# Optimization experiments

Measured on AMD Instinct MI355X. Metric: run time of the kernel, lower is better.

## Reference

```python
import jax, jax.numpy as jnp
import numpy as np

N = 100000   # nodes
E = 1600000  # edges
F_IN = 64    # n_features
H = 32       # hidden_size
OUT = 1      # output_size


def _lin(k, fan_in, fan_out):
    return (jax.random.normal(k, (fan_in, fan_out), jnp.float32) / np.sqrt(fan_in)).astype(jnp.float32)


def setup_inputs() -> dict:
    key = jax.random.key(0)
    ks = jax.random.split(key, 16)
    x = jax.random.normal(ks[0], (N, F_IN), jnp.float32)
    edge_index = jax.random.randint(ks[1], (2, E), 0, N, dtype=jnp.int64)
    # guarantee current_node (=0) has outgoing edges so the legal-move mask is non-empty
    edge_index = edge_index.at[0, :64].set(0)
    edge_attr = jax.random.uniform(ks[2], (E,), jnp.float32)
    return {
        "x": x, "edge_index": edge_index, "edge_attr": edge_attr, "current_node": 0,
        # conv_in: GraphConv(F_IN -> H)
        "Win_rel": _lin(ks[3], F_IN, H), "bin_rel": jnp.zeros((H,), jnp.float32), "Win_root": _lin(ks[4], F_IN, H),
        # conv_hidden: GraphConv(H -> H)
        "Wh_rel": _lin(ks[5], H, H), "bh_rel": jnp.zeros((H,), jnp.float32), "Wh_root": _lin(ks[6], H, H),
        # policy_conv: GraphConv(H -> OUT)
        "Wp_rel": _lin(ks[7], H, OUT), "bp_rel": jnp.zeros((OUT,), jnp.float32), "Wp_root": _lin(ks[8], H, OUT),
        # value_conv: GraphConv(H -> OUT)
        "Wv_rel": _lin(ks[9], H, OUT), "bv_rel": jnp.zeros((OUT,), jnp.float32), "Wv_root": _lin(ks[10], H, OUT),
    }


def _graph_conv(h, src, dst, ew, W_rel, b_rel, W_root):
    # PyG GraphConv: out_i = W_root h_i + W_rel * sum_{j->i} e_ji * h_j + b
    msg = h[src] * ew[:, None]                              # [E, d] gather + scale
    agg = jax.ops.segment_sum(msg, dst, num_segments=N)      # [N, d] scatter-add
    return agg @ W_rel + b_rel + h @ W_root


def reference(x, edge_index, edge_attr, current_node,
              Win_rel, bin_rel, Win_root,
              Wh_rel, bh_rel, Wh_root,
              Wp_rel, bp_rel, Wp_root,
              Wv_rel, bv_rel, Wv_root):
    src, dst = edge_index[0], edge_index[1]
    h = jax.nn.relu(_graph_conv(x, src, dst, edge_attr, Win_rel, bin_rel, Win_root))
    h = jax.nn.relu(_graph_conv(h, src, dst, edge_attr, Wh_rel, bh_rel, Wh_root))
    p = _graph_conv(h, src, dst, edge_attr, Wp_rel, bp_rel, Wp_root)  # [N, 1]
    v = _graph_conv(h, src, dst, edge_attr, Wv_rel, bv_rel, Wv_root)  # [N, 1]
    # illegal_moves_mask: 1 for nodes directly reachable from current_node
    hit = (src == current_node).astype(jnp.float32)
    mask = (jnp.zeros((N,), jnp.float32).at[dst].add(hit) > 0).astype(jnp.float32)
    p_m = mask * p.T                                   # [1, N]
    p_m = jnp.where(p_m == 0, -jnp.inf, p_m)
    p_soft = jax.nn.softmax(p_m, axis=1)
    v_m = mask * v.T                                   # [1, N]
    return p_soft.reshape(-1), v_m.reshape(-1)
```

## Files before the change

kernel.cpp:

```cpp
#include <hip/hip_runtime.h>
#include <hip/hip_fp16.h>
#include <cmath>

static constexpr int NN = 100000;
static constexpr int NE = 1600000;
static const size_t NW = (size_t)NN * 32;
static constexpr int SUB = 256;
static constexpr int NSUB = 391;
static constexpr int CH = 8192;
static constexpr int NCH = (NE + CH - 1) / CH;
static constexpr int BCAP = 5200;
static constexpr int CSRN = NSUB * BCAP;
static constexpr int MCAP = 4096;

__device__ __forceinline__ float ent_w(unsigned e)
{
    return __half2float(__ushort_as_half((unsigned short)(e >> 17)));
}
__device__ __forceinline__ int ent_s(unsigned e)
{
    int s = (int)(e & 0x1FFFF);
    return s < NN ? s : NN - 1;
}

__device__ __forceinline__ float4 pack8(const float* v)
{
    union { __half2 h2[4]; float4 f4; } u;
    u.h2[0] = __floats2half2_rn(v[0], v[1]);
    u.h2[1] = __floats2half2_rn(v[2], v[3]);
    u.h2[2] = __floats2half2_rn(v[4], v[5]);
    u.h2[3] = __floats2half2_rn(v[6], v[7]);
    return u.f4;
}

__device__ __forceinline__ int wave_incl_scan(int v, int lane)
{
    int s = v;
#pragma unroll
    for (int d = 1; d < 64; d <<= 1) {
        int o = __shfl_up(s, d, 64);
        if (lane >= d) s += o;
    }
    return s;
}

__global__ void __launch_bounds__(512) fused_build_mm1_k(
    const int* __restrict__ src, const int* __restrict__ dst,
    const float* __restrict__ ew, const int* __restrict__ curp,
    int* __restrict__ maskb, int* __restrict__ mcount, int* __restrict__ mlist,
    int* __restrict__ bcnt, unsigned* __restrict__ bx,
    unsigned char* __restrict__ bd,
    const float* __restrict__ x, const float* __restrict__ Wrel,
    const float* __restrict__ Wroot, const float* __restrict__ bin,
    __half* __restrict__ proj1, __half* __restrict__ root1)
{
    __shared__ union {
        struct {
            unsigned sBufX[CH];
            unsigned char sBufD[CH];
            int lhist[NSUB];
            int lpos[NSUB];
            int lstart[NSUB];
            int lbase[NSUB];
            int tscan[512];
        } s;
        struct {
            float sX[128 * 65];
            float sW[64 * 68];
        } m;
    } u;

    int t = threadIdx.x;
    int bid = blockIdx.x;

    if (bid < NCH) {
        for (int i = t; i < NSUB; i += 512) { u.s.lhist[i] = 0; u.s.lpos[i] = 0; }
        __syncthreads();
        int c0 = bid * CH;
        int cur = curp[0];
        unsigned rx[CH / 512];
        int rd[CH / 512];
#pragma unroll
        for (int it = 0; it < CH / 512; ++it) {
            int e = c0 + it * 512 + t;
            rd[it] = -1;
            if (e < NE) {
                int d = dst[e];
                int sv = src[e];
                if ((unsigned)d < (unsigned)NN) {
                    rd[it] = d;
                    unsigned bits = __half_as_ushort(__float2half(ew[e]));
                    rx[it] = ((unsigned)sv & 0x1FFFF) | (bits << 17);
                    atomicAdd(&u.s.lhist[d >> 8], 1);
                    if (sv == cur) {
                        if (atomicExch(maskb + d, 1) == 0) {
                            int idx = atomicAdd(mcount, 1);
                            if (idx < MCAP) mlist[idx] = d;
                        }
                    }
                }
            }
        }
        __syncthreads();
        {
            int v = (t < NSUB) ? u.s.lhist[t] : 0;
            int lane = t & 63, wv = t >> 6;
            int sI = wave_incl_scan(v, lane);
            if (lane == 63) u.s.tscan[wv] = sI;
            __syncthreads();
            if (t == 0) {
                int r = 0;
#pragma unroll
                for (int w2 = 0; w2 < 8; ++w2) {
                    int xw = u.s.tscan[w2];
                    u.s.tscan[8 + w2] = r;
                    r += xw;
                }
            }
            __syncthreads();
            if (t < NSUB) {
                u.s.lstart[t] = sI + u.s.tscan[8 + wv] - v;
                u.s.lbase[t] = (v > 0) ? atomicAdd(&bcnt[t], v) : 0;
            }
        }
        __syncthreads();
#pragma unroll
        for (int it = 0; it < CH / 512; ++it) {
            if (rd[it] >= 0) {
                int b = rd[it] >> 8;
                int p = atomicAdd(&u.s.lpos[b], 1);
                int pos = u.s.lstart[b] + p;
                u.s.sBufX[pos] = rx[it];
                u.s.sBufD[pos] = (unsigned char)(rd[it] & 255);
            }
        }
        __syncthreads();
        int grp = t >> 4, l16 = t & 15;
        for (int b = grp; b < NSUB; b += 32) {
            int s0 = u.s.lstart[b];
            int cb = u.s.lhist[b];
            int gb = u.s.lbase[b];
            size_t gb0 = (size_t)b * BCAP;
            for (int j = l16; j < cb; j += 16) {
                unsigned pos = (unsigned)(gb + j);
                if (pos < (unsigned)BCAP) {
                    bx[gb0 + pos] = u.s.sBufX[s0 + j];
                    bd[gb0 + pos] = u.s.sBufD[s0 + j];
                }
            }
        }
    } else {
        int mb = bid - NCH;
        for (int i = t; i < 64 * 32; i += 512) {
            int k = i >> 5, j = i & 31;
            u.m.sW[k * 68 + j] = Wrel[i];
            u.m.sW[k * 68 + 32 + j] = Wroot[i];
        }
        int base = mb * 128;
        for (int i = t; i < 2048; i += 512) {
            int node = i >> 4;
            int k = (i & 15) * 4;
            int n = base + node;
            if (n >= NN) n = NN - 1;
            float4 v4 = *(const float4*)(x + (size_t)n * 64 + k);
            float* p = u.m.sX + node * 65 + k;
            p[0] = v4.x; p[1] = v4.y; p[2] = v4.z; p[3] = v4.w;
        }
        __syncthreads();
        int cg = t & 7;
        int ng = t >> 3;
        int c0m = 8 * cg;
        float acc[2][8] = {};
        for (int k = 0; k < 64; ++k) {
            float xv0 = u.m.sX[(2 * ng + 0) * 65 + k];
            float xv1 = u.m.sX[(2 * ng + 1) * 65 + k];
            float4 w0 = *(const float4*)(u.m.sW + k * 68 + c0m);
            float4 w1 = *(const float4*)(u.m.sW + k * 68 + c0m + 4);
            const float* wp = (const float*)&w0;
#pragma unroll
            for (int j = 0; j < 4; ++j) {
                float w = wp[j];
                acc[0][j] = fmaf(xv0, w, acc[0][j]);
                acc[1][j] = fmaf(xv1, w, acc[1][j]);
            }
            const float* wq = (const float*)&w1;
#pragma unroll
            for (int j = 0; j < 4; ++j) {
                float w = wq[j];
                acc[0][4 + j] = fmaf(xv0, w, acc[0][4 + j]);
                acc[1][4 + j] = fmaf(xv1, w, acc[1][4 + j]);
            }
        }
#pragma unroll
        for (int r = 0; r < 2; ++r) {
            int n = base + 2 * ng + r;
            if (n >= NN) break;
            if (cg < 4) {
                *(float4*)(proj1 + (size_t)n * 32 + c0m) = pack8(acc[r]);
            } else {
                int c = c0m - 32;
                float vv[8];
#pragma unroll
                for (int j = 0; j < 8; ++j) vv[j] = acc[r][j] + bin[c + j];
                *(float4*)(root1 + (size_t)n * 32 + c) = pack8(vv);
            }
        }
    }
}

__global__ void __launch_bounds__(1024) sortagg1_k(
    const unsigned* __restrict__ bx, const unsigned char* __restrict__ bd,
    const int* __restrict__ bcnt,
    const __half* __restrict__ proj1, const __half* __restrict__ root1,
    unsigned* __restrict__ csr4, int* __restrict__ deg, int* __restrict__ off,
    __half* __restrict__ h1)
{
    __shared__ unsigned sX[BCAP];
    __shared__ unsigned char sD[BCAP];
    __shared__ unsigned sE[BCAP];
    __shared__ int lhist[SUB];
    __shared__ int lstart[SUB];
    __shared__ int lcur[SUB];
    __shared__ int tscan[16];
    int g = blockIdx.x, t = threadIdx.x;
    if (t < SUB) { lhist[t] = 0; lcur[t] = 0; }
    __syncthreads();
    int cnt = bcnt[g];
    if (cnt < 0) cnt = 0;
    if (cnt > BCAP) cnt = BCAP;
    size_t gbase = (size_t)g * BCAP;
    for (int i = t; i < cnt; i += 1024) {
        unsigned e = bx[gbase + i];
        unsigned char d = bd[gbase + i];
        sX[i] = e;
        sD[i] = d;
        atomicAdd(&lhist[d], 1);
    }
    __syncthreads();
    {
        int v = (t < SUB) ? lhist[t] : 0;
        int lane = t & 63, wv = t >> 6;
        int sI = wave_incl_scan(v, lane);
        if (t < SUB && lane == 63) tscan[wv] = sI;
        __syncthreads();
        if (t == 0) {
            int r = 0;
#pragma unroll
            for (int w2 = 0; w2 < 4; ++w2) {
                int xw = tscan[w2];
                tscan[8 + w2] = r;
                r += xw;
            }
        }
        __syncthreads();
        if (t < SUB) lstart[t] = sI + tscan[8 + wv] - v;
    }
    __syncthreads();
    for (int i = t; i < cnt; i += 1024) {
        int ld = (int)sD[i];
        int p = atomicAdd(&lcur[ld], 1);
        int pos = lstart[ld] + p;
        if ((unsigned)pos < (unsigned)BCAP) sE[pos] = sX[i];
    }
    __syncthreads();
    int base = g * BCAP;
    if (t < SUB) {
        int n = g * SUB + t;
        if (n < NN) {
            deg[n] = lhist[t];
            off[n] = base + lstart[t];
        }
    }
    for (int i = t; i < cnt; i += 1024) {
        unsigned pos = (unsigned)(base + i);
        if (pos < (unsigned)CSRN) csr4[pos] = sE[i];
    }
    int q = t & 3;
    int f0 = q * 8;
    int l = t >> 2;
    int n = g * SUB + l;
    if (n >= NN) return;
    int st = lstart[l];
    int dg = lhist[l];
    if (st < 0) st = 0;
    if (st > BCAP) st = BCAP;
    if (dg < 0) dg = 0;
    if (dg > BCAP - st) dg = BCAP - st;
    float acc[8] = {0.f, 0.f, 0.f, 0.f, 0.f, 0.f, 0.f, 0.f};
    int i = 0;
    for (; i + 1 < dg; i += 2) {
        unsigned e0 = sE[st + i];
        unsigned e1 = sE[st + i + 1];
        float w0 = ent_w(e0), w1 = ent_w(e1);
        float4 r0 = *(const float4*)(proj1 + (size_t)ent_s(e0) * 32 + f0);
        float4 r1 = *(const float4*)(proj1 + (size_t)ent_s(e1) * 32 + f0);
        const __half2* h0 = (const __half2*)&r0;
        const __half2* h1p = (const __half2*)&r1;
#pragma unroll
        for (int u = 0; u < 4; ++u) {
            float2 a = __half22float2(h0[u]);
            float2 b = __half22float2(h1p[u]);
            acc[2 * u] = fmaf(w0, a.x, acc[2 * u]);
            acc[2 * u + 1] = fmaf(w0, a.y, acc[2 * u + 1]);
            acc[2 * u] = fmaf(w1, b.x, acc[2 * u]);
            acc[2 * u + 1] = fmaf(w1, b.y, acc[2 * u + 1]);
        }
    }
    if (i < dg) {
        unsigned e0 = sE[st + i];
        float w0 = ent_w(e0);
        float4 r0 = *(const float4*)(proj1 + (size_t)ent_s(e0) * 32 + f0);
        const __half2* h0 = (const __half2*)&r0;
#pragma unroll
        for (int u = 0; u < 4; ++u) {
            float2 a = __half22float2(h0[u]);
            acc[2 * u] = fmaf(w0, a.x, acc[2 * u]);
            acc[2 * u + 1] = fmaf(w0, a.y, acc[2 * u + 1]);
        }
    }
    float4 rr = *(const float4*)(root1 + (size_t)n * 32 + f0);
    const __half2* rp = (const __half2*)&rr;
    float h[8];
#pragma unroll
    for (int u = 0; u < 4; ++u) {
        float2 f2 = __half22float2(rp[u]);
        h[2 * u] = fmaxf(acc[2 * u] + f2.x, 0.f);
        h[2 * u + 1] = fmaxf(acc[2 * u + 1] + f2.y, 0.f);
    }
    *(float4*)(h1 + (size_t)n * 32 + f0) = pack8(h);
}

__global__ void __launch_bounds__(256) mm2_k(
    const __half* __restrict__ h1, const float* __restrict__ Wrel,
    const float* __restrict__ Wroot, const float* __restrict__ bh,
    __half* __restrict__ proj2, __half* __restrict__ root2)
{
    __shared__ float sX[128 * 33];
    __shared__ float sW[32 * 68];
    int t = threadIdx.x;
    for (int i = t; i < 32 * 32; i += 256) {
        int k = i >> 5, j = i & 31;
        sW[k * 68 + j] = Wrel[i];
        sW[k * 68 + 32 + j] = Wroot[i];
    }
    int base = blockIdx.x * 128;
    for (int i = t; i < 512; i += 256) {
        int node = i >> 2;
        int hs = (i & 3) * 8;
        int n = base + node;
        if (n >= NN) n = NN - 1;
        float4 v = *(const float4*)(h1 + (size_t)n * 32 + hs);
        const __half2* hp = (const __half2*)&v;
        float* p = sX + node * 33 + hs;
#pragma unroll
        for (int u = 0; u < 4; ++u) {
            float2 f2 = __half22float2(hp[u]);
            p[2 * u] = f2.x;
            p[2 * u + 1] = f2.y;
        }
    }
    __syncthreads();
    int cg = t & 7;
    int ng = t >> 3;
    int c0 = 8 * cg;
    float acc[4][8] = {};
    for (int k = 0; k < 32; ++k) {
        float xv0 = sX[(4 * ng + 0) * 33 + k];
        float xv1 = sX[(4 * ng + 1) * 33 + k];
        float xv2 = sX[(4 * ng + 2) * 33 + k];
        float xv3 = sX[(4 * ng + 3) * 33 + k];
        float4 w0 = *(const float4*)(sW + k * 68 + c0);
        float4 w1 = *(const float4*)(sW + k * 68 + c0 + 4);
        const float* wp = (const float*)&w0;
#pragma unroll
        for (int j = 0; j < 4; ++j) {
            float w = wp[j];
            acc[0][j] = fmaf(xv0, w, acc[0][j]);
            acc[1][j] = fmaf(xv1, w, acc[1][j]);
            acc[2][j] = fmaf(xv2, w, acc[2][j]);
            acc[3][j] = fmaf(xv3, w, acc[3][j]);
        }
        const float* wq = (const float*)&w1;
#pragma unroll
        for (int j = 0; j < 4; ++j) {
            float w = wq[j];
            acc[0][4 + j] = fmaf(xv0, w, acc[0][4 + j]);
            acc[1][4 + j] = fmaf(xv1, w, acc[1][4 + j]);
            acc[2][4 + j] = fmaf(xv2, w, acc[2][4 + j]);
            acc[3][4 + j] = fmaf(xv3, w, acc[3][4 + j]);
        }
    }
#pragma unroll
    for (int r = 0; r < 4; ++r) {
        int n = base + 4 * ng + r;
        if (n >= NN) break;
        if (cg < 4) {
            *(float4*)(proj2 + (size_t)n * 32 + c0) = pack8(acc[r]);
        } else {
            int c = c0 - 32;
            float v[8];
#pragma unroll
            for (int j = 0; j < 8; ++j) v[j] = acc[r][j] + bh[c + j];
            *(float4*)(root2 + (size_t)n * 32 + c) = pack8(v);
        }
    }
}

__global__ void __launch_bounds__(256) agg2_v4(
    const __half* __restrict__ proj2, const __half* __restrict__ root2,
    const float* __restrict__ Wp_rel, const float* __restrict__ Wp_root,
    const float* __restrict__ bp, const float* __restrict__ Wv_rel,
    const float* __restrict__ Wv_root, const float* __restrict__ bv,
    const unsigned* __restrict__ csr4, const int* __restrict__ off,
    const int* __restrict__ deg, float2* __restrict__ pv,
    float* __restrict__ pbase, float* __restrict__ vbase,
    float* __restrict__ out_p, float* __restrict__ out_v)
{
    __shared__ float sHead[4 * 32];
    if (threadIdx.x < 32) {
        sHead[threadIdx.x] = Wp_rel[threadIdx.x];
        sHead[32 + threadIdx.x] = Wp_root[threadIdx.x];
        sHead[64 + threadIdx.x] = Wv_rel[threadIdx.x];
        sHead[96 + threadIdx.x] = Wv_root[threadIdx.x];
    }
    __syncthreads();
    int t = threadIdx.x;
    int q = t & 3;
    int f0 = q * 8;
    int n = blockIdx.x * 64 + (t >> 2);
    if (n >= NN) return;
    int st = off[n];
    int dg = deg[n];
    if (st < 0) st = 0;
    if (st > CSRN) st = CSRN;
    if (dg < 0) dg = 0;
    if (dg > CSRN - st) dg = CSRN - st;
    float acc[8] = {0.f, 0.f, 0.f, 0.f, 0.f, 0.f, 0.f, 0.f};
    int i = 0;
    for (; i + 3 < dg; i += 4) {
        unsigned e0 = csr4[st + i];
        unsigned e1 = csr4[st + i + 1];
        unsigned e2 = csr4[st + i + 2];
        unsigned e3 = csr4[st + i + 3];
        float4 r0 = *(const float4*)(proj2 + (size_t)ent_s(e0) * 32 + f0);
        float4 r1 = *(const float4*)(proj2 + (size_t)ent_s(e1) * 32 + f0);
        float4 r2 = *(const float4*)(proj2 + (size_t)ent_s(e2) * 32 + f0);
        float4 r3 = *(const float4*)(proj2 + (size_t)ent_s(e3) * 32 + f0);
        float w0 = ent_w(e0), w1 = ent_w(e1), w2 = ent_w(e2), w3 = ent_w(e3);
        const __half2* h0 = (const __half2*)&r0;
        const __half2* h1p = (const __half2*)&r1;
        const __half2* h2p = (const __half2*)&r2;
        const __half2* h3p = (const __half2*)&r3;
#pragma unroll
        for (int u = 0; u < 4; ++u) {
            float2 a = __half22float2(h0[u]);
            float2 b = __half22float2(h1p[u]);
            float2 c = __half22float2(h2p[u]);
            float2 d = __half22float2(h3p[u]);
            acc[2 * u]     = fmaf(w0, a.x, acc[2 * u]);
            acc[2 * u + 1] = fmaf(w0, a.y, acc[2 * u + 1]);
            acc[2 * u]     = fmaf(w1, b.x, acc[2 * u]);
            acc[2 * u + 1] = fmaf(w1, b.y, acc[2 * u + 1]);
            acc[2 * u]     = fmaf(w2, c.x, acc[2 * u]);
            acc[2 * u + 1] = fmaf(w2, c.y, acc[2 * u + 1]);
            acc[2 * u]     = fmaf(w3, d.x, acc[2 * u]);
            acc[2 * u + 1] = fmaf(w3, d.y, acc[2 * u + 1]);
        }
    }
    for (; i < dg; ++i) {
        unsigned e0 = csr4[st + i];
        float w0 = ent_w(e0);
        float4 r0 = *(const float4*)(proj2 + (size_t)ent_s(e0) * 32 + f0);
        const __half2* h0 = (const __half2*)&r0;
#pragma unroll
        for (int u = 0; u < 4; ++u) {
            float2 a = __half22float2(h0[u]);
            acc[2 * u] = fmaf(w0, a.x, acc[2 * u]);
            acc[2 * u + 1] = fmaf(w0, a.y, acc[2 * u + 1]);
        }
    }
    float4 rr = *(const float4*)(root2 + (size_t)n * 32 + f0);
    const __half2* rp = (const __half2*)&rr;
    float h[8];
#pragma unroll
    for (int u = 0; u < 4; ++u) {
        float2 f2 = __half22float2(rp[u]);
        h[2 * u] = fmaxf(acc[2 * u] + f2.x, 0.f);
        h[2 * u + 1] = fmaxf(acc[2 * u + 1] + f2.y, 0.f);
    }
    float prv = 0.f, pov = 0.f, vrv = 0.f, vov = 0.f;
#pragma unroll
    for (int j = 0; j < 8; ++j) {
        prv = fmaf(h[j], sHead[f0 + j], prv);
        pov = fmaf(h[j], sHead[32 + f0 + j], pov);
        vrv = fmaf(h[j], sHead[64 + f0 + j], vrv);
        vov = fmaf(h[j], sHead[96 + f0 + j], vov);
    }
#pragma unroll
    for (int m = 1; m <= 2; m <<= 1) {
        prv += __shfl_xor(prv, m, 64);
        pov += __shfl_xor(pov, m, 64);
        vrv += __shfl_xor(vrv, m, 64);
        vov += __shfl_xor(vov, m, 64);
    }
    if (q == 0) {
        pv[n] = make_float2(prv, vrv);
        pbase[n] = pov + bp[0];
        vbase[n] = vov + bv[0];
        out_p[n] = 0.f;
        out_v[n] = 0.f;
    }
}

__global__ void __launch_bounds__(256) masked_softmax_k(
    const int* __restrict__ mlist, const int* __restrict__ mcount,
    const unsigned* __restrict__ csr4, const int* __restrict__ off,
    const int* __restrict__ deg, const float2* __restrict__ pv,
    const float* __restrict__ pbase, const float* __restrict__ vbase,
    float* __restrict__ out_p, float* __restrict__ out_v)
{
    __shared__ float sPm[MCAP];
    __shared__ float sV[MCAP];
    __shared__ int sN[MCAP];
    __shared__ float sMx, sSum;
    __shared__ float sred[4];
    int m = mcount[0];
    if (m > MCAP) m = MCAP;
    if (m < 0) m = 0;
    int lane4 = threadIdx.x & 3;
    for (int idx = threadIdx.x >> 2; idx < m; idx += 64) {
        int n = mlist[idx];
        if ((unsigned)n >= (unsigned)NN) n = 0;
        int st = off[n];
        int dg = deg[n];
        if (st < 0) st = 0;
        if (st > CSRN) st = CSRN;
        if (dg < 0) dg = 0;
        if (dg > CSRN - st) dg = CSRN - st;
        float pa = 0.f, va = 0.f;
        for (int i = lane4; i < dg; i += 4) {
            unsigned ent = csr4[st + i];
            int s = ent_s(ent);
            float w = ent_w(ent);
            float2 tv = pv[s];
            pa = fmaf(tv.x, w, pa);
            va = fmaf(tv.y, w, va);
        }
        pa += __shfl_xor(pa, 1, 64);
        pa += __shfl_xor(pa, 2, 64);
        va += __shfl_xor(va, 1, 64);
        va += __shfl_xor(va, 2, 64);
        if (lane4 == 0) {
            sN[idx] = n;
            float p = pa + pbase[n];
            sPm[idx] = (p == 0.f) ? -INFINITY : p;
            sV[idx] = va + vbase[n];
        }
    }
    __syncthreads();
    float mx = -INFINITY;
    for (int i = threadIdx.x; i < m; i += 256) mx = fmaxf(mx, sPm[i]);
#pragma unroll
    for (int k = 32; k; k >>= 1) mx = fmaxf(mx, __shfl_xor(mx, k, 64));
    if ((threadIdx.x & 63) == 0) sred[threadIdx.x >> 6] = mx;
    __syncthreads();
    if (threadIdx.x == 0)
        sMx = fmaxf(fmaxf(sred[0], sred[1]), fmaxf(sred[2], sred[3]));
    __syncthreads();
    float sum = 0.f;
    for (int i = threadIdx.x; i < m; i += 256) {
        float x = sPm[i];
        sum += (x == -INFINITY) ? 0.f : expf(x - sMx);
    }
#pragma unroll
    for (int k = 32; k; k >>= 1) sum += __shfl_xor(sum, k, 64);
    if ((threadIdx.x & 63) == 0) sred[threadIdx.x >> 6] = sum;
    __syncthreads();
    if (threadIdx.x == 0) sSum = sred[0] + sred[1] + sred[2] + sred[3];
    __syncthreads();
    for (int idx = threadIdx.x; idx < m; idx += 256) {
        int n = sN[idx];
        float x = sPm[idx];
        out_p[n] = (x == -INFINITY) ? 0.f : expf(x - sMx) / sSum;
        out_v[n] = sV[idx];
    }
}

extern "C" void kernel_launch(void* const* d_in, const int* in_sizes, int n_in,
                              void* d_out, int out_size, void* d_ws,
                              size_t ws_size, hipStream_t stream)
{
    const float* x        = (const float*)d_in[0];
    const int*   ei       = (const int*)d_in[1];
    const float* ew       = (const float*)d_in[2];
    const int*   cur      = (const int*)d_in[3];
    const float* Win_rel  = (const float*)d_in[4];
    const float* bin_rel  = (const float*)d_in[5];
    const float* Win_root = (const float*)d_in[6];
    const float* Wh_rel   = (const float*)d_in[7];
    const float* bh_rel   = (const float*)d_in[8];
    const float* Wh_root  = (const float*)d_in[9];
    const float* Wp_rel   = (const float*)d_in[10];
    const float* bp       = (const float*)d_in[11];
    const float* Wp_root  = (const float*)d_in[12];
    const float* Wv_rel   = (const float*)d_in[13];
    const float* bv       = (const float*)d_in[14];
    const float* Wv_root  = (const float*)d_in[15];

    const int* srcA = ei;
    const int* dstA = ei + NE;

    char* w8 = (char*)d_ws;
    unsigned* csr4 = (unsigned*)w8;
    int* deg    = (int*)(csr4 + CSRN);
    int* off    = deg + NN;
    int* maskb  = off + NN;
    int* mcount = maskb + NN;
    int* bcnt   = mcount + 8;
    int* mlist  = bcnt + 400;
    __half* proj1 = (__half*)(mlist + MCAP);
    __half* root1 = proj1 + NW;
    __half* h1    = root1 + NW;
    __half* proj2 = h1 + NW;
    __half* root2 = proj2 + NW;
    float2* pv    = (float2*)(root2 + NW);
    float* pbase  = (float*)(pv + NN);
    float* vbase  = pbase + NN;
    unsigned* bucket_x = (unsigned*)(vbase + NN);
    unsigned char* bucket_d = (unsigned char*)(bucket_x + CSRN);

    float* out_p = (float*)d_out;
    float* out_v = out_p + NN;

    const int NB_MM    = (NN + 127) / 128;
    const int NB_AGG   = (NN + 63) / 64;
    const int NB_FUSED = NCH + NB_MM;

    hipMemsetAsync(maskb, 0, ((size_t)NN + 8 + 400) * sizeof(int), stream);

    fused_build_mm1_k<<<NB_FUSED, 512, 0, stream>>>(
        srcA, dstA, ew, cur, maskb, mcount, mlist, bcnt, bucket_x, bucket_d,
        x, Win_rel, Win_root, bin_rel, proj1, root1);
    sortagg1_k<<<NSUB, 1024, 0, stream>>>(bucket_x, bucket_d, bcnt,
                                          proj1, root1, csr4, deg, off, h1);
    mm2_k<<<NB_MM, 256, 0, stream>>>(h1, Wh_rel, Wh_root, bh_rel, proj2, root2);
    agg2_v4<<<NB_AGG, 256, 0, stream>>>(proj2, root2, Wp_rel, Wp_root, bp,
                                        Wv_rel, Wv_root, bv, csr4, off, deg,
                                        pv, pbase, vbase, out_p, out_v);
    masked_softmax_k<<<1, 256, 0, stream>>>(mlist, mcount, csr4, off, deg, pv,
                                            pbase, vbase, out_p, out_v);
}
```

Baseline: 226.1 us.

## Compute layer-2 aggregation only for nodes needed by the masked output

During the sort step, the code marks the masked nodes and their in-neighbours and collects them into a compact need list. The second aggregation and head kernel then runs only over that list instead of all nodes, and the outputs are zeroed with a memset. This is exact because unmasked nodes output zero and masked nodes only depend on these neighbours' h2. It adds atomic dedup work inside sortagg1 and caps the list at 8192 entries, which could overflow if the mask were larger.

```diff
diff --git a/kernel.cpp b/kernel.cpp
--- a/kernel.cpp
+++ b/kernel.cpp
@@ -12,6 +12,7 @@
 static constexpr int BCAP = 5200;
 static constexpr int CSRN = NSUB * BCAP;
 static constexpr int MCAP = 4096;
+static constexpr int NCAP = 8192;
 
 __device__ __forceinline__ float ent_w(unsigned e)
 {
@@ -210,7 +211,9 @@
 
 __global__ void __launch_bounds__(1024) sortagg1_k(
     const unsigned* __restrict__ bx, const unsigned char* __restrict__ bd,
-    const int* __restrict__ bcnt,
+    const int* __restrict__ bcnt, const int* __restrict__ maskb,
+    int* __restrict__ needb, int* __restrict__ ncount,
+    int* __restrict__ needlist,
     const __half* __restrict__ proj1, const __half* __restrict__ root1,
     unsigned* __restrict__ csr4, int* __restrict__ deg, int* __restrict__ off,
     __half* __restrict__ h1)
@@ -269,6 +272,20 @@
         if (n < NN) {
             deg[n] = lhist[t];
             off[n] = base + lstart[t];
+            if (maskb[n] != 0) {
+                if (atomicExch(needb + n, 1) == 0) {
+                    int ix = atomicAdd(ncount, 1);
+                    if (ix < NCAP) needlist[ix] = n;
+                }
+                int s0 = lstart[t], dgn = lhist[t];
+                for (int i2 = 0; i2 < dgn; ++i2) {
+                    int s = ent_s(sE[s0 + i2]);
+                    if (atomicExch(needb + s, 1) == 0) {
+                        int ix = atomicAdd(ncount, 1);
+                        if (ix < NCAP) needlist[ix] = s;
+                    }
+                }
+            }
         }
     }
     for (int i = t; i < cnt; i += 1024) {
@@ -406,15 +423,15 @@
     }
 }
 
-__global__ void __launch_bounds__(256) agg2_v4(
+__global__ void __launch_bounds__(256) need_gather_k(
     const __half* __restrict__ proj2, const __half* __restrict__ root2,
     const float* __restrict__ Wp_rel, const float* __restrict__ Wp_root,
     const float* __restrict__ bp, const float* __restrict__ Wv_rel,
     const float* __restrict__ Wv_root, const float* __restrict__ bv,
     const unsigned* __restrict__ csr4, const int* __restrict__ off,
-    const int* __restrict__ deg, float2* __restrict__ pv,
-    float* __restrict__ pbase, float* __restrict__ vbase,
-    float* __restrict__ out_p, float* __restrict__ out_v)
+    const int* __restrict__ deg, const int* __restrict__ needlist,
+    const int* __restrict__ ncount, float2* __restrict__ pv,
+    float* __restrict__ pbase, float* __restrict__ vbase)
 {
     __shared__ float sHead[4 * 32];
     if (threadIdx.x < 32) {
@@ -427,8 +444,12 @@
     int t = threadIdx.x;
     int q = t & 3;
     int f0 = q * 8;
-    int n = blockIdx.x * 64 + (t >> 2);
-    if (n >= NN) return;
+    int m = ncount[0];
+    if (m > NCAP) m = NCAP;
+    int idx = blockIdx.x * 64 + (t >> 2);
+    if (idx >= m) return;
+    int n = needlist[idx];
+    if ((unsigned)n >= (unsigned)NN) n = 0;
     int st = off[n];
     int dg = deg[n];
     if (st < 0) st = 0;
@@ -497,18 +518,16 @@
         vov = fmaf(h[j], sHead[96 + f0 + j], vov);
     }
 #pragma unroll
-    for (int m = 1; m <= 2; m <<= 1) {
-        prv += __shfl_xor(prv, m, 64);
-        pov += __shfl_xor(pov, m, 64);
-        vrv += __shfl_xor(vrv, m, 64);
-        vov += __shfl_xor(vov, m, 64);
+    for (int mm = 1; mm <= 2; mm <<= 1) {
+        prv += __shfl_xor(prv, mm, 64);
+        pov += __shfl_xor(pov, mm, 64);
+        vrv += __shfl_xor(vrv, mm, 64);
+        vov += __shfl_xor(vov, mm, 64);
     }
     if (q == 0) {
         pv[n] = make_float2(prv, vrv);
         pbase[n] = pov + bp[0];
         vbase[n] = vov + bv[0];
-        out_p[n] = 0.f;
-        out_v[n] = 0.f;
     }
 }
 
@@ -617,8 +636,11 @@
     int* maskb  = off + NN;
     int* mcount = maskb + NN;
     int* bcnt   = mcount + 8;
-    int* mlist  = bcnt + 400;
-    __half* proj1 = (__half*)(mlist + MCAP);
+    int* needb  = bcnt + 400;
+    int* ncnt   = needb + NN;
+    int* mlist  = ncnt + 8;
+    int* needlist = mlist + MCAP;
+    __half* proj1 = (__half*)(needlist + NCAP);
     __half* root1 = proj1 + NW;
     __half* h1    = root1 + NW;
     __half* proj2 = h1 + NW;
@@ -633,20 +655,22 @@
     float* out_v = out_p + NN;
 
     const int NB_MM    = (NN + 127) / 128;
-    const int NB_AGG   = (NN + 63) / 64;
     const int NB_FUSED = NCH + NB_MM;
-
-    hipMemsetAsync(maskb, 0, ((size_t)NN + 8 + 400) * sizeof(int), stream);
+    const int NB_NEED  = NCAP / 64;
+
+    hipMemsetAsync(maskb, 0, ((size_t)2 * NN + 416) * sizeof(int), stream);
+    hipMemsetAsync(d_out, 0, 2 * (size_t)NN * sizeof(float), stream);
 
     fused_build_mm1_k<<<NB_FUSED, 512, 0, stream>>>(
         srcA, dstA, ew, cur, maskb, mcount, mlist, bcnt, bucket_x, bucket_d,
         x, Win_rel, Win_root, bin_rel, proj1, root1);
-    sortagg1_k<<<NSUB, 1024, 0, stream>>>(bucket_x, bucket_d, bcnt,
+    sortagg1_k<<<NSUB, 1024, 0, stream>>>(bucket_x, bucket_d, bcnt, maskb,
+                                          needb, ncnt, needlist,
                                           proj1, root1, csr4, deg, off, h1);
     mm2_k<<<NB_MM, 256, 0, stream>>>(h1, Wh_rel, Wh_root, bh_rel, proj2, root2);
-    agg2_v4<<<NB_AGG, 256, 0, stream>>>(proj2, root2, Wp_rel, Wp_root, bp,
-                                        Wv_rel, Wv_root, bv, csr4, off, deg,
-                                        pv, pbase, vbase, out_p, out_v);
+    need_gather_k<<<NB_NEED, 256, 0, stream>>>(
+        proj2, root2, Wp_rel, Wp_root, bp, Wv_rel, Wv_root, bv,
+        csr4, off, deg, needlist, ncnt, pv, pbase, vbase);
     masked_softmax_k<<<1, 256, 0, stream>>>(mlist, mcount, csr4, off, deg, pv,
                                             pbase, vbase, out_p, out_v);
 }
```

Result: faster. 214.9 us (-5.0%).
